# Performance work log

Hardware: AMD Instinct MI355X
Metric: run time of the kernel (lower is better)

Reference implementation:

```python
import jax, jax.numpy as jnp
import numpy as np

DIM = 1024
NUM_HEADS = 16
HEAD_DIM = 64  # DIM // NUM_HEADS
BATCH = 2
SEQ = 2048


def setup_inputs() -> dict:
    key = jax.random.key(0)
    ks = jax.random.split(key, 6)
    x = jax.random.normal(ks[0], (BATCH, SEQ, DIM), dtype=jnp.float32)
    # Linear weights stored as [in, out] so y = x @ W (same math as torch Linear).
    Wq = jax.random.normal(ks[1], (DIM, DIM), dtype=jnp.float32) * (DIM ** -0.5)
    # MQA: single shared KV head of size HEAD_DIM.
    Wk = jax.random.normal(ks[2], (DIM, HEAD_DIM), dtype=jnp.float32) * (DIM ** -0.5)
    Wv = jax.random.normal(ks[3], (DIM, HEAD_DIM), dtype=jnp.float32) * (DIM ** -0.5)
    Wo = jax.random.normal(ks[4], (DIM, DIM), dtype=jnp.float32) * (DIM ** -0.5)
    bo = jax.random.normal(ks[5], (DIM,), dtype=jnp.float32) * 0.01
    return {"x": x, "Wq": Wq, "Wk": Wk, "Wv": Wv, "Wo": Wo, "bo": bo}


def reference(x, Wq, Wk, Wv, Wo, bo):
    b, s, _ = x.shape
    scale = HEAD_DIM ** -0.5
    # Per-head queries [b, h, s, d]
    q = (x @ Wq).reshape(b, s, NUM_HEADS, HEAD_DIM).transpose(0, 2, 1, 3) * scale
    # Shared single KV head [b, s, d]
    k = x @ Wk
    v = x @ Wv
    # Materialized scores [b, h, s_q, s_k]
    scores = jnp.einsum('bhqd,bkd->bhqk', q, k)
    causal = jnp.tril(jnp.ones((s, s), dtype=bool))  # True where allowed
    scores = jnp.where(causal, scores, -jnp.inf)
    # Manual stable softmax (max, exp, sum, div) as in the original
    max_scores = jnp.max(scores, axis=-1, keepdims=True)
    exp_scores = jnp.exp(scores - max_scores)
    attn = exp_scores / jnp.sum(exp_scores, axis=-1, keepdims=True)
    out = jnp.einsum('bhqk,bkd->bhqd', attn, v)  # [b, h, s, d]
    out = out.transpose(0, 2, 1, 3).reshape(b, s, DIM)
    return out @ Wo + bo
```

## Files before the change

### kernel.cpp

```cpp
#include <hip/hip_runtime.h>

typedef unsigned short u16;
typedef __attribute__((ext_vector_type(8))) short short8;
typedef __attribute__((ext_vector_type(4))) float f32x4;

static __device__ __forceinline__ u16 f32_to_bf16(float f) {
  unsigned u = __float_as_uint(f);
  u += 0x7fffu + ((u >> 16) & 1u);
  return (u16)(u >> 16);
}

static __device__ __forceinline__ unsigned cvt_pk_bf16(float a, float b) {
  unsigned r;
  asm("v_cvt_pk_bf16_f32 %0, %1, %2" : "=v"(r) : "v"(a), "v"(b));
  return r;
}

static __device__ __forceinline__ void async16(u16* lds, const u16* g) {
  __builtin_amdgcn_global_load_lds(
      (const __attribute__((address_space(1))) void*)g,
      (__attribute__((address_space(3))) void*)lds, 16, 0, 0);
}


__global__ void __launch_bounds__(256) prep_kernel(
    const float* __restrict__ x,
    const float* __restrict__ Wq, const float* __restrict__ Wk,
    const float* __restrict__ Wv, const float* __restrict__ Wo,
    u16* __restrict__ Xb, u16* __restrict__ WqT, u16* __restrict__ WkvT,
    u16* __restrict__ WoT) {
  __shared__ u16 T[64][72];
  int id = blockIdx.x;
  int tid = threadIdx.x;
  if (id < 2048) {
    int base = (id * 256 + tid) * 8;
    float4 a = *(const float4*)&x[base];
    float4 b = *(const float4*)&x[base + 4];
    short8 v;
    v[0] = (short)f32_to_bf16(a.x); v[1] = (short)f32_to_bf16(a.y);
    v[2] = (short)f32_to_bf16(a.z); v[3] = (short)f32_to_bf16(a.w);
    v[4] = (short)f32_to_bf16(b.x); v[5] = (short)f32_to_bf16(b.y);
    v[6] = (short)f32_to_bf16(b.z); v[7] = (short)f32_to_bf16(b.w);
    *(short8*)&Xb[base] = v;
    return;
  }
  int id2 = id - 2048;
  const float* src; u16* dst; int tk, tn, src_ld, row_off;
  if (id2 < 256)      { src = Wq; dst = WqT;  tk = id2 & 15; tn = id2 >> 4; src_ld = 1024; row_off = 0; }
  else if (id2 < 512) { int i = id2 - 256; src = Wo; dst = WoT; tk = i & 15; tn = i >> 4; src_ld = 1024; row_off = 0; }
  else if (id2 < 528) { src = Wk; dst = WkvT; tk = id2 - 512; tn = 0; src_ld = 64; row_off = 0; }
  else                { src = Wv; dst = WkvT; tk = id2 - 528; tn = 0; src_ld = 64; row_off = 64; }
  int k0 = tk * 64, n0 = tn * 64;
#pragma unroll
  for (int it = 0; it < 2; ++it) {
    int c = tid + it * 256;
    int r = c >> 3, cc = (c & 7) * 8;
    const float* p = &src[(k0 + r) * src_ld + n0 + cc];
    float4 a = *(const float4*)&p[0];
    float4 b = *(const float4*)&p[4];
    short8 v;
    v[0] = (short)f32_to_bf16(a.x); v[1] = (short)f32_to_bf16(a.y);
    v[2] = (short)f32_to_bf16(a.z); v[3] = (short)f32_to_bf16(a.w);
    v[4] = (short)f32_to_bf16(b.x); v[5] = (short)f32_to_bf16(b.y);
    v[6] = (short)f32_to_bf16(b.z); v[7] = (short)f32_to_bf16(b.w);
    *(short8*)&T[r][cc] = v;
  }
  __syncthreads();
#pragma unroll
  for (int it = 0; it < 2; ++it) {
    int c = tid + it * 256;
    int r = c >> 3, cc = (c & 7) * 8;
    short8 v;
#pragma unroll
    for (int j = 0; j < 8; ++j) v[j] = (short)T[cc + j][r];
    *(short8*)&dst[(row_off + n0 + r) * 1024 + k0 + cc] = v;
  }
}

__device__ __forceinline__ void stage_64x128(
    const u16* __restrict__ A, const u16* __restrict__ BT, int m0, int K,
    int k0, u16* As, u16* Bs, int w, int lrow, int swz8) {
#pragma unroll
  for (int it = 0; it < 2; ++it) {
    int W = w * 2 + it;
    async16(As + W * 512, &A[(size_t)(m0 + W * 8 + lrow) * K + k0 + swz8]);
  }
#pragma unroll
  for (int it = 0; it < 4; ++it) {
    int W = w * 4 + it;
    async16(Bs + W * 512, &BT[(size_t)(W * 8 + lrow) * K + k0 + swz8]);
  }
}

__device__ __forceinline__ void gemm_core_64x128_db(
    const u16* __restrict__ A, const u16* __restrict__ BT, int m0, int K,
    f32x4 (&acc)[2][4], u16* As, u16* Bs,
    int lane, int w, int wr, int wc, int g, int lo) {
  int lrow = lane >> 3;
  int swz8 = ((lane & 7) ^ lrow) * 8;
  int lo7 = lo & 7;
  const int NK = K >> 6;
  stage_64x128(A, BT, m0, K, 0, As, Bs, w, lrow, swz8);
  for (int kt = 0; kt < NK; ++kt) {
    int cur = kt & 1;
    __syncthreads();
    if (kt + 1 < NK)
      stage_64x128(A, BT, m0, K, (kt + 1) * 64,
                   As + (cur ^ 1) * 4096, Bs + (cur ^ 1) * 8192, w, lrow, swz8);
    const u16* Asc = As + cur * 4096;
    const u16* Bsc = Bs + cur * 8192;
#pragma unroll
    for (int ks = 0; ks < 2; ++ks) {
      int pc = ((ks * 4 + g) ^ lo7) * 8;
      short8 af[2], bf[4];
#pragma unroll
      for (int i = 0; i < 2; ++i)
        af[i] = *(const short8*)&Asc[(wr * 32 + i * 16 + lo) * 64 + pc];
#pragma unroll
      for (int i = 0; i < 4; ++i)
        bf[i] = *(const short8*)&Bsc[(wc * 64 + i * 16 + lo) * 64 + pc];
#pragma unroll
      for (int mi = 0; mi < 2; ++mi)
#pragma unroll
        for (int ni = 0; ni < 4; ++ni)
          acc[mi][ni] = __builtin_amdgcn_mfma_f32_16x16x32_bf16(
              af[mi], bf[ni], acc[mi][ni], 0, 0, 0);
    }
  }
}

__global__ void __launch_bounds__(256) qkv_gemm(
    const u16* __restrict__ Xb, const u16* __restrict__ WqT,
    const u16* __restrict__ WkvT, u16* __restrict__ Qb, u16* __restrict__ KVb,
    u16* __restrict__ VTb) {
  __shared__ u16 As[2 * 64 * 64];
  __shared__ u16 Bs[2 * 128 * 64];
  int tid = threadIdx.x, lane = tid & 63, w = tid >> 6;
  int wr = w >> 1, wc = w & 1, g = lane >> 4, lo = lane & 15;
  int m0 = blockIdx.x * 64, nb = blockIdx.y;
  const u16* BT = (nb < 8) ? (WqT + (size_t)nb * 128 * 1024) : WkvT;
  f32x4 acc[2][4];
  f32x4 zz = {0.f, 0.f, 0.f, 0.f};
#pragma unroll
  for (int i = 0; i < 2; ++i)
#pragma unroll
    for (int j = 0; j < 4; ++j) acc[i][j] = zz;
  gemm_core_64x128_db(Xb, BT, m0, 1024, acc, As, Bs, lane, w, wr, wc, g, lo);
#pragma unroll
  for (int mi = 0; mi < 2; ++mi)
#pragma unroll
    for (int ni = 0; ni < 4; ++ni)
#pragma unroll
      for (int r = 0; r < 4; ++r) {
        int row = m0 + wr * 32 + mi * 16 + g * 4 + r;
        int col = wc * 64 + ni * 16 + lo;
        u16 v = f32_to_bf16(acc[mi][ni][r]);
        if (nb < 8) {
          Qb[row * 1024 + nb * 128 + col] = v;
        } else if (wc == 0) {
          KVb[row * 64 + col] = v;
        } else {
          int d = col - 64;
          VTb[(((row >> 11) * 64) + d) * 2048 + (row & 2047)] = v;
        }
      }
}

__global__ void __launch_bounds__(256, 4) attn_kernel(
    const u16* __restrict__ Qb, const u16* __restrict__ KVb,
    const u16* __restrict__ VTb, u16* __restrict__ AOb) {
  __shared__ u16 Ks[2][64 * 64];
  __shared__ u16 Vt[2][64 * 64];
  __shared__ u16 Ps[4][16][64];
  int tid = threadIdx.x, lane = tid & 63, w = tid >> 6;
  int gq = lane >> 4, lo = lane & 15;
  int h = blockIdx.y;
  int b = blockIdx.z;
  int a = (blockIdx.x + (h & 8) + (b << 4)) & 31;
  int qb = a * 64 + w * 16;
  int lrow = lane >> 3;
  int swz8 = ((lane & 7) ^ lrow) * 8;
  int lo7 = lo & 7;

  short8 qf[2];
  {
    const u16* qp = &Qb[(size_t)(b * 2048 + qb + lo) * 1024 + h * 64];
    qf[0] = *(const short8*)&qp[gq * 8];
    qf[1] = *(const short8*)&qp[32 + gq * 8];
  }

  f32x4 zz = {0.f, 0.f, 0.f, 0.f};
  f32x4 oacc[4];
#pragma unroll
  for (int i = 0; i < 4; ++i) oacc[i] = zz;
  float lsum = 0.f;

  const float kExp = 0.18033688011112042f;
  const float kOff = 11.541560327111707f;

  auto stage_kv = [&](int t, int bu) {
#pragma unroll
    for (int it = 0; it < 2; ++it) {
      int W = w * 2 + it;
      async16(&Ks[bu][W * 512],
              &KVb[(size_t)(b * 2048 + t * 64 + W * 8 + lrow) * 64 + swz8]);
      async16(&Vt[bu][W * 512],
              &VTb[((size_t)b * 64 + W * 8 + lrow) * 2048 + t * 64 + swz8]);
    }
  };

  int nst = a + 1;
  stage_kv(0, 0);
  for (int t = 0; t < nst; ++t) {
    int cur = t & 1;
    __syncthreads();
    if (t + 1 < nst) stage_kv(t + 1, cur ^ 1);
    const u16* Kc = Ks[cur];
    const u16* Vc = Vt[cur];

    f32x4 sacc[4];
#pragma unroll
    for (int ns = 0; ns < 4; ++ns) sacc[ns] = zz;
#pragma unroll
    for (int ks = 0; ks < 2; ++ks) {
      int pc = ((ks * 4 + gq) ^ lo7) * 8;
      short8 kf[4];
#pragma unroll
      for (int ns = 0; ns < 4; ++ns)
        kf[ns] = *(const short8*)&Kc[(ns * 16 + lo) * 64 + pc];
#pragma unroll
      for (int ns = 0; ns < 4; ++ns)
        sacc[ns] = __builtin_amdgcn_mfma_f32_16x16x32_bf16(
            kf[ns], qf[ks], sacc[ns], 0, 0, 0);
    }

    bool diag = (t == a);
    int qg = qb + lo;
#pragma unroll
    for (int ns = 0; ns < 4; ++ns) {
      float p[4];
#pragma unroll
      for (int r = 0; r < 4; ++r) {
        float pv = __builtin_amdgcn_exp2f(fmaf(sacc[ns][r], kExp, -kOff));
        if (diag) {
          int kg = t * 64 + ns * 16 + gq * 4 + r;
          if (kg > qg) pv = 0.f;
        }
        lsum += pv;
        p[r] = pv;
      }
      uint2 pd;
      pd.x = cvt_pk_bf16(p[0], p[1]);
      pd.y = cvt_pk_bf16(p[2], p[3]);
      int ch = (2 * ns + (gq >> 1)) ^ lo7;
      *(uint2*)&Ps[w][lo][ch * 8 + (gq & 1) * 4] = pd;
    }
    __threadfence_block();

#pragma unroll
    for (int k2 = 0; k2 < 2; ++k2) {
      int pc = ((k2 * 4 + gq) ^ lo7) * 8;
      short8 pf = *(const short8*)&Ps[w][lo][pc];
      short8 vf[4];
#pragma unroll
      for (int ds = 0; ds < 4; ++ds)
        vf[ds] = *(const short8*)&Vc[(ds * 16 + lo) * 64 + pc];
#pragma unroll
      for (int ds = 0; ds < 4; ++ds)
        oacc[ds] = __builtin_amdgcn_mfma_f32_16x16x32_bf16(
            vf[ds], pf, oacc[ds], 0, 0, 0);
    }
  }

  lsum += __shfl_xor(lsum, 16);
  lsum += __shfl_xor(lsum, 32);
  float inv = 1.0f / lsum;
  int row = b * 2048 + qb + lo;
#pragma unroll
  for (int ds = 0; ds < 4; ++ds) {
    uint2 od;
    od.x = cvt_pk_bf16(oacc[ds][0] * inv, oacc[ds][1] * inv);
    od.y = cvt_pk_bf16(oacc[ds][2] * inv, oacc[ds][3] * inv);
    *(uint2*)&AOb[(size_t)row * 1024 + h * 64 + ds * 16 + gq * 4] = od;
  }
}

__global__ void __launch_bounds__(256) out_gemm(
    const u16* __restrict__ A, const u16* __restrict__ WoT,
    const float* __restrict__ bias, float* __restrict__ C) {
  __shared__ u16 As[2 * 64 * 64];
  __shared__ u16 Bs[2 * 128 * 64];
  int tid = threadIdx.x, lane = tid & 63, w = tid >> 6;
  int wr = w >> 1, wc = w & 1, g = lane >> 4, lo = lane & 15;
  int m0 = blockIdx.x * 64, nb = blockIdx.y;
  const u16* BT = WoT + (size_t)nb * 128 * 1024;
  f32x4 acc[2][4];
  f32x4 zz = {0.f, 0.f, 0.f, 0.f};
#pragma unroll
  for (int i = 0; i < 2; ++i)
#pragma unroll
    for (int j = 0; j < 4; ++j) acc[i][j] = zz;
  gemm_core_64x128_db(A, BT, m0, 1024, acc, As, Bs, lane, w, wr, wc, g, lo);
#pragma unroll
  for (int mi = 0; mi < 2; ++mi)
#pragma unroll
    for (int ni = 0; ni < 4; ++ni)
#pragma unroll
      for (int r = 0; r < 4; ++r) {
        int row = m0 + wr * 32 + mi * 16 + g * 4 + r;
        int col = nb * 128 + wc * 64 + ni * 16 + lo;
        C[row * 1024 + col] = acc[mi][ni][r] + bias[col];
      }
}

extern "C" void kernel_launch(void* const* d_in, const int* in_sizes, int n_in,
                              void* d_out, int out_size, void* d_ws, size_t ws_size,
                              hipStream_t stream) {
  const float* x  = (const float*)d_in[0];
  const float* Wq = (const float*)d_in[1];
  const float* Wk = (const float*)d_in[2];
  const float* Wv = (const float*)d_in[3];
  const float* Wo = (const float*)d_in[4];
  const float* bo = (const float*)d_in[5];
  float* out = (float*)d_out;

  u16* ws   = (u16*)d_ws;
  u16* AOb  = ws;
  u16* KVb  = AOb + 4194304;
  u16* VTb  = KVb + 262144;
  u16* Xb   = VTb + 262144;
  u16* WqT  = Xb + 4194304;
  u16* WoT  = WqT + 1048576;
  u16* WkvT = WoT + 1048576;
  u16* Qb   = (u16*)d_out;

  prep_kernel<<<2592, 256, 0, stream>>>(x, Wq, Wk, Wv, Wo, Xb, WqT, WkvT, WoT);
  qkv_gemm<<<dim3(64, 9), 256, 0, stream>>>(Xb, WqT, WkvT, Qb, KVb, VTb);
  attn_kernel<<<dim3(32, 16, 2), 256, 0, stream>>>(Qb, KVb, VTb, AOb);
  out_gemm<<<dim3(64, 8), 256, 0, stream>>>(AOb, WoT, bo, out);
}
```

Before: 156.2 us.

## Process two heads per attention block and stage 128-key KV tiles

Each attention block now handles two query heads that share the single MQA KV head, so every K/V tile loaded into LDS feeds twice as many MFMAs. The KV staging tile grows from 64 to 128 keys per iteration, which halves the number of barriers, and the causal block order is rebalanced by reversing it for batch 1. The cost is more LDS and registers per block (launch bounds drop from 4 to 2 waves per SIMD) and half as many blocks in the grid, which lowers occupancy and parallelism.

```diff
diff --git a/kernel.cpp b/kernel.cpp
--- a/kernel.cpp
+++ b/kernel.cpp
@@ -166,122 +166,147 @@
       }
 }
 
-__global__ void __launch_bounds__(256, 4) attn_kernel(
+__global__ void __launch_bounds__(256, 2) attn_kernel(
     const u16* __restrict__ Qb, const u16* __restrict__ KVb,
     const u16* __restrict__ VTb, u16* __restrict__ AOb) {
-  __shared__ u16 Ks[2][64 * 64];
-  __shared__ u16 Vt[2][64 * 64];
-  __shared__ u16 Ps[4][16][64];
+  __shared__ u16 Ks[2][128 * 64];
+  __shared__ u16 Vt[2][2][64 * 64];
+  __shared__ u16 Ps[4][2][16][64];
   int tid = threadIdx.x, lane = tid & 63, w = tid >> 6;
   int gq = lane >> 4, lo = lane & 15;
-  int h = blockIdx.y;
+  int hg = blockIdx.y;
   int b = blockIdx.z;
-  int a = (blockIdx.x + (h & 8) + (b << 4)) & 31;
+  int a = b ? (31 - (int)blockIdx.x) : (int)blockIdx.x;
   int qb = a * 64 + w * 16;
   int lrow = lane >> 3;
   int swz8 = ((lane & 7) ^ lrow) * 8;
   int lo7 = lo & 7;
 
-  short8 qf[2];
-  {
-    const u16* qp = &Qb[(size_t)(b * 2048 + qb + lo) * 1024 + h * 64];
-    qf[0] = *(const short8*)&qp[gq * 8];
-    qf[1] = *(const short8*)&qp[32 + gq * 8];
+  short8 qf[2][2];
+#pragma unroll
+  for (int h = 0; h < 2; ++h) {
+    const u16* qp = &Qb[(size_t)(b * 2048 + qb + lo) * 1024 + (hg * 2 + h) * 64];
+    qf[h][0] = *(const short8*)&qp[gq * 8];
+    qf[h][1] = *(const short8*)&qp[32 + gq * 8];
   }
 
   f32x4 zz = {0.f, 0.f, 0.f, 0.f};
-  f32x4 oacc[4];
-#pragma unroll
-  for (int i = 0; i < 4; ++i) oacc[i] = zz;
-  float lsum = 0.f;
+  f32x4 oacc[2][4];
+  float lsum[2] = {0.f, 0.f};
+#pragma unroll
+  for (int h = 0; h < 2; ++h)
+#pragma unroll
+    for (int i = 0; i < 4; ++i) oacc[h][i] = zz;
 
   const float kExp = 0.18033688011112042f;
   const float kOff = 11.541560327111707f;
 
   auto stage_kv = [&](int t, int bu) {
 #pragma unroll
-    for (int it = 0; it < 2; ++it) {
-      int W = w * 2 + it;
-      async16(&Ks[bu][W * 512],
-              &KVb[(size_t)(b * 2048 + t * 64 + W * 8 + lrow) * 64 + swz8]);
-      async16(&Vt[bu][W * 512],
-              &VTb[((size_t)b * 64 + W * 8 + lrow) * 2048 + t * 64 + swz8]);
+    for (int it = 0; it < 4; ++it) {
+      int seg = w * 4 + it;
+      async16(&Ks[bu][seg * 512],
+              &KVb[(size_t)(b * 2048 + t * 128 + seg * 8 + lrow) * 64 + swz8]);
+      int kk = seg >> 3, s2 = seg & 7;
+      async16(&Vt[bu][kk][s2 * 512],
+              &VTb[((size_t)b * 64 + s2 * 8 + lrow) * 2048 + t * 128 + kk * 64 + swz8]);
     }
   };
 
-  int nst = a + 1;
+  int nst = (a >> 1) + 1;
   stage_kv(0, 0);
   for (int t = 0; t < nst; ++t) {
     int cur = t & 1;
     __syncthreads();
     if (t + 1 < nst) stage_kv(t + 1, cur ^ 1);
-    const u16* Kc = Ks[cur];
-    const u16* Vc = Vt[cur];
-
-    f32x4 sacc[4];
-#pragma unroll
-    for (int ns = 0; ns < 4; ++ns) sacc[ns] = zz;
-#pragma unroll
-    for (int ks = 0; ks < 2; ++ks) {
-      int pc = ((ks * 4 + gq) ^ lo7) * 8;
-      short8 kf[4];
-#pragma unroll
-      for (int ns = 0; ns < 4; ++ns)
-        kf[ns] = *(const short8*)&Kc[(ns * 16 + lo) * 64 + pc];
-#pragma unroll
-      for (int ns = 0; ns < 4; ++ns)
-        sacc[ns] = __builtin_amdgcn_mfma_f32_16x16x32_bf16(
-            kf[ns], qf[ks], sacc[ns], 0, 0, 0);
+#pragma unroll
+    for (int kk = 0; kk < 2; ++kk) {
+      int kt = 2 * t + kk;
+      if (kt <= a) {
+        const u16* Kck = &Ks[cur][kk * 4096];
+        const u16* Vc = Vt[cur][kk];
+
+        f32x4 sacc[2][4];
+#pragma unroll
+        for (int h = 0; h < 2; ++h)
+#pragma unroll
+          for (int ns = 0; ns < 4; ++ns) sacc[h][ns] = zz;
+#pragma unroll
+        for (int ks = 0; ks < 2; ++ks) {
+          int pc = ((ks * 4 + gq) ^ lo7) * 8;
+          short8 kf[4];
+#pragma unroll
+          for (int ns = 0; ns < 4; ++ns)
+            kf[ns] = *(const short8*)&Kck[(ns * 16 + lo) * 64 + pc];
+#pragma unroll
+          for (int ns = 0; ns < 4; ++ns)
+#pragma unroll
+            for (int h = 0; h < 2; ++h)
+              sacc[h][ns] = __builtin_amdgcn_mfma_f32_16x16x32_bf16(
+                  kf[ns], qf[h][ks], sacc[h][ns], 0, 0, 0);
+        }
+
+        bool diag = (kt == a);
+        int qg = qb + lo;
+#pragma unroll
+        for (int h = 0; h < 2; ++h)
+#pragma unroll
+          for (int ns = 0; ns < 4; ++ns) {
+            float p[4];
+#pragma unroll
+            for (int r = 0; r < 4; ++r) {
+              float pv = __builtin_amdgcn_exp2f(fmaf(sacc[h][ns][r], kExp, -kOff));
+              if (diag) {
+                int kg = kt * 64 + ns * 16 + gq * 4 + r;
+                if (kg > qg) pv = 0.f;
+              }
+              lsum[h] += pv;
+              p[r] = pv;
+            }
+            uint2 pd;
+            pd.x = cvt_pk_bf16(p[0], p[1]);
+            pd.y = cvt_pk_bf16(p[2], p[3]);
+            int ch = (2 * ns + (gq >> 1)) ^ lo7;
+            *(uint2*)&Ps[w][h][lo][ch * 8 + (gq & 1) * 4] = pd;
+          }
+        __threadfence_block();
+
+#pragma unroll
+        for (int k2 = 0; k2 < 2; ++k2) {
+          int pc = ((k2 * 4 + gq) ^ lo7) * 8;
+          short8 vf[4];
+#pragma unroll
+          for (int ds = 0; ds < 4; ++ds)
+            vf[ds] = *(const short8*)&Vc[(ds * 16 + lo) * 64 + pc];
+          short8 pf[2];
+#pragma unroll
+          for (int h = 0; h < 2; ++h)
+            pf[h] = *(const short8*)&Ps[w][h][lo][pc];
+#pragma unroll
+          for (int h = 0; h < 2; ++h)
+#pragma unroll
+            for (int ds = 0; ds < 4; ++ds)
+              oacc[h][ds] = __builtin_amdgcn_mfma_f32_16x16x32_bf16(
+                  vf[ds], pf[h], oacc[h][ds], 0, 0, 0);
+        }
+      }
     }
-
-    bool diag = (t == a);
-    int qg = qb + lo;
-#pragma unroll
-    for (int ns = 0; ns < 4; ++ns) {
-      float p[4];
-#pragma unroll
-      for (int r = 0; r < 4; ++r) {
-        float pv = __builtin_amdgcn_exp2f(fmaf(sacc[ns][r], kExp, -kOff));
-        if (diag) {
-          int kg = t * 64 + ns * 16 + gq * 4 + r;
-          if (kg > qg) pv = 0.f;
-        }
-        lsum += pv;
-        p[r] = pv;
-      }
-      uint2 pd;
-      pd.x = cvt_pk_bf16(p[0], p[1]);
-      pd.y = cvt_pk_bf16(p[2], p[3]);
-      int ch = (2 * ns + (gq >> 1)) ^ lo7;
-      *(uint2*)&Ps[w][lo][ch * 8 + (gq & 1) * 4] = pd;
+  }
+
+  int row = b * 2048 + qb + lo;
+#pragma unroll
+  for (int h = 0; h < 2; ++h) {
+    float ls = lsum[h];
+    ls += __shfl_xor(ls, 16);
+    ls += __shfl_xor(ls, 32);
+    float inv = 1.0f / ls;
+#pragma unroll
+    for (int ds = 0; ds < 4; ++ds) {
+      uint2 od;
+      od.x = cvt_pk_bf16(oacc[h][ds][0] * inv, oacc[h][ds][1] * inv);
+      od.y = cvt_pk_bf16(oacc[h][ds][2] * inv, oacc[h][ds][3] * inv);
+      *(uint2*)&AOb[(size_t)row * 1024 + (hg * 2 + h) * 64 + ds * 16 + gq * 4] = od;
     }
-    __threadfence_block();
-
-#pragma unroll
-    for (int k2 = 0; k2 < 2; ++k2) {
-      int pc = ((k2 * 4 + gq) ^ lo7) * 8;
-      short8 pf = *(const short8*)&Ps[w][lo][pc];
-      short8 vf[4];
-#pragma unroll
-      for (int ds = 0; ds < 4; ++ds)
-        vf[ds] = *(const short8*)&Vc[(ds * 16 + lo) * 64 + pc];
-#pragma unroll
-      for (int ds = 0; ds < 4; ++ds)
-        oacc[ds] = __builtin_amdgcn_mfma_f32_16x16x32_bf16(
-            vf[ds], pf, oacc[ds], 0, 0, 0);
-    }
-  }
-
-  lsum += __shfl_xor(lsum, 16);
-  lsum += __shfl_xor(lsum, 32);
-  float inv = 1.0f / lsum;
-  int row = b * 2048 + qb + lo;
-#pragma unroll
-  for (int ds = 0; ds < 4; ++ds) {
-    uint2 od;
-    od.x = cvt_pk_bf16(oacc[ds][0] * inv, oacc[ds][1] * inv);
-    od.y = cvt_pk_bf16(oacc[ds][2] * inv, oacc[ds][3] * inv);
-    *(uint2*)&AOb[(size_t)row * 1024 + h * 64 + ds * 16 + gq * 4] = od;
   }
 }
 
@@ -336,6 +361,6 @@
 
   prep_kernel<<<2592, 256, 0, stream>>>(x, Wq, Wk, Wv, Wo, Xb, WqT, WkvT, WoT);
   qkv_gemm<<<dim3(64, 9), 256, 0, stream>>>(Xb, WqT, WkvT, Qb, KVb, VTb);
-  attn_kernel<<<dim3(32, 16, 2), 256, 0, stream>>>(Qb, KVb, VTb, AOb);
+  attn_kernel<<<dim3(32, 8, 2), 256, 0, stream>>>(Qb, KVb, VTb, AOb);
   out_gemm<<<dim3(64, 8), 256, 0, stream>>>(AOb, WoT, bo, out);
 }
```

New measurement: 159.3 us. About the same (+2.0%).
